# Optimization experiments

Hardware: AMD Instinct MI355X
Metric: run time of the kernel (lower is better)

The kernel has to match this reference:

```python
import jax, jax.numpy as jnp
import numpy as np

HEADS = 16
MAX_DIST = 1024

def setup_inputs() -> dict:
    key = jax.random.key(0)
    k1, k2, k3, k4 = jax.random.split(key, 4)
    b, n, dim = 2, 2048, 1024
    x = jax.random.normal(k1, (b, n, dim), dtype=jnp.float32)
    W_qkv = jax.random.normal(k2, (3 * dim, dim), dtype=jnp.float32) * (dim ** -0.5)
    W_out = jax.random.normal(k3, (dim, dim), dtype=jnp.float32) * (dim ** -0.5)
    b_out = jnp.zeros((dim,), dtype=jnp.float32)
    rel_emb = jax.random.normal(k4, (2 * MAX_DIST + 1, HEADS), dtype=jnp.float32) * 0.02
    return {"x": x, "W_qkv": W_qkv, "W_out": W_out, "b_out": b_out, "rel_emb": rel_emb}

def reference(x, W_qkv, W_out, b_out, rel_emb):
    b, n, dim = x.shape
    h = HEADS
    d = dim // h
    scale = d ** -0.5
    qkv = jnp.einsum('bnd,ed->bne', x, W_qkv)  # [b, n, 3*dim]
    q, k, v = jnp.split(qkv, 3, axis=-1)
    def to_heads(t):
        return t.reshape(b, n, h, d).transpose(0, 2, 1, 3)  # b h n d
    q, k, v = to_heads(q), to_heads(k), to_heads(v)
    # relative position bias: [1, h, n, n]
    dist = jnp.arange(n)[None, :] - jnp.arange(n)[:, None]
    idx = jnp.clip(dist, -MAX_DIST, MAX_DIST) + MAX_DIST  # [n, n]
    rel_bias = rel_emb[idx].transpose(2, 0, 1)[None]  # [1, h, n, n]
    scores = jnp.einsum('bhqd,bhkd->bhqk', q, k) * scale + rel_bias
    attn = jax.nn.softmax(scores, axis=-1)
    out = jnp.einsum('bhqk,bhkd->bhqd', attn, v)
    out = out.transpose(0, 2, 1, 3).reshape(b, n, dim)
    return jnp.einsum('bnd,ed->bne', out, W_out) + b_out
```

## Files before the change

### kernel.cpp

```cpp
#include <hip/hip_runtime.h>
#include <hip/hip_bf16.h>

typedef __attribute__((ext_vector_type(8))) short short8;
typedef __attribute__((ext_vector_type(4))) float f32x4;
typedef __attribute__((ext_vector_type(16))) float f32x16;
typedef float f32x4u __attribute__((ext_vector_type(4), aligned(4)));
typedef __attribute__((ext_vector_type(4))) unsigned short u16x4;
typedef __attribute__((ext_vector_type(2))) unsigned int u32x2;
typedef __attribute__((ext_vector_type(4))) unsigned int u32x4;
typedef __hip_bfloat16 bf16;

#define SCALE_Q 0.18033688f

#define GLD_LDS16(g, l) __builtin_amdgcn_global_load_lds(                      \
    (const __attribute__((address_space(1))) void*)(g),                        \
    (__attribute__((address_space(3))) void*)(l), 16, 0, 0)

static __device__ __forceinline__ f32x4 mfma16(short8 a, short8 b, f32x4 c) {
  return __builtin_amdgcn_mfma_f32_16x16x32_bf16(a, b, c, 0, 0, 0);
}
static __device__ __forceinline__ f32x16 mfma32(short8 a, short8 b, f32x16 c) {
  return __builtin_amdgcn_mfma_f32_32x32x16_bf16(a, b, c, 0, 0, 0);
}

static __device__ __forceinline__ unsigned cvtpk(float lo, float hi) {
  unsigned r;
  asm("v_cvt_pk_bf16_f32 %0, %1, %2" : "=v"(r) : "v"(lo), "v"(hi));
  return r;
}

static __device__ __forceinline__ float fexp2(float x) {
  float r;
  asm("v_exp_f32 %0, %1" : "=v"(r) : "v"(x));
  return r;
}

#define PLSWAP(a, b) asm("v_permlane32_swap_b32 %0, %1" : "+v"(a), "+v"(b))

__global__ __launch_bounds__(256) void k_pre(
    const float* __restrict__ x, const float* __restrict__ Wqkv,
    const float* __restrict__ Wout, const float* __restrict__ rel,
    bf16* __restrict__ xb, bf16* __restrict__ wqb, bf16* __restrict__ wob,
    float* __restrict__ relpf) {
  int bid = blockIdx.x;
  if (bid < 8192) {
    const float* in;
    bf16* out;
    long i;
    if (bid < 4096) {
      in = x; out = xb; i = (long)bid * 256 + threadIdx.x;
    } else if (bid < 7168) {
      in = Wqkv; out = wqb; i = (long)(bid - 4096) * 256 + threadIdx.x;
    } else {
      in = Wout; out = wob; i = (long)(bid - 7168) * 256 + threadIdx.x;
    }
    f32x4 v = *(const f32x4*)(in + i * 4);
    u16x4 o;
#pragma unroll
    for (int j = 0; j < 4; ++j)
      o[j] = __builtin_bit_cast(unsigned short, __float2bfloat16(v[j]));
    *(u16x4*)((unsigned short*)out + i * 4) = o;
  } else {
    int base = (bid - 8192) * 1024 + threadIdx.x;
#pragma unroll
    for (int k = 0; k < 4; ++k) {
      int i = base + k * 256;
      int h = i >> 12, ii = i & 4095;
      int dd = ii - 2047;
      dd = dd < -1024 ? -1024 : (dd > 1024 ? 1024 : dd);
      relpf[i] = rel[(size_t)(dd + 1024) * 16 + h] * 1.44269504f - 16.0f;
    }
  }
}

__global__ __launch_bounds__(256, 3) void k_gemm(
    const bf16* __restrict__ A, const bf16* __restrict__ B,
    int M, int N, int K, int epi,
    bf16* __restrict__ Qb, bf16* __restrict__ Kb, bf16* __restrict__ Vt,
    float* __restrict__ Out, const float* __restrict__ bias) {
  __shared__ bf16 lA[3][4096];
  __shared__ bf16 lB[3][4096];
  const int tid = threadIdx.x, w = tid >> 6, l = tid & 63;
  const int m0 = blockIdx.x * 128, n0 = blockIdx.y * 128;
  const int wrow = (w >> 1) * 64, wcol = (w & 1) * 64;
  const int fr = l & 15, fq = l >> 4;
  f32x4 acc[4][4] = {};
  const int c0 = w * 64 + l, c1 = c0 + 256;
  const bf16* Ag0 = A + (size_t)(m0 + (c0 >> 2)) * K + (c0 & 3) * 8;
  const bf16* Ag1 = A + (size_t)(m0 + (c1 >> 2)) * K + (c1 & 3) * 8;
  const bf16* Bg0 = B + (size_t)(n0 + (c0 >> 2)) * K + (c0 & 3) * 8;
  const bf16* Bg1 = B + (size_t)(n0 + (c1 >> 2)) * K + (c1 & 3) * 8;
  bf16* lA0 = &lA[0][w * 512];
  bf16* lA1 = &lA[0][2048 + w * 512];
  bf16* lB0 = &lB[0][w * 512];
  bf16* lB1 = &lB[0][2048 + w * 512];

#define GSTAGE(T, BI)                                                          \
  do {                                                                         \
    const int ko_ = (T) * 32;                                                  \
    GLD_LDS16(Ag0 + ko_, lA0 + (BI) * 4096);                                   \
    GLD_LDS16(Ag1 + ko_, lA1 + (BI) * 4096);                                   \
    GLD_LDS16(Bg0 + ko_, lB0 + (BI) * 4096);                                   \
    GLD_LDS16(Bg1 + ko_, lB1 + (BI) * 4096);                                   \
  } while (0)

  const int nk = K >> 5;
  GSTAGE(0, 0);
  __builtin_amdgcn_sched_barrier(0);
  GSTAGE(1, 1);
  __builtin_amdgcn_sched_barrier(0);

  int bc_ = 0, bs_ = 2;
  for (int t = 0; t < nk; ++t) {
    asm volatile("s_waitcnt vmcnt(4)" ::: "memory");
    __builtin_amdgcn_s_barrier();
    __builtin_amdgcn_sched_barrier(0);
    int tt = (t + 2 < nk) ? t + 2 : nk - 1;
    GSTAGE(tt, bs_);
    __builtin_amdgcn_sched_barrier(0);
    const bf16* pA = &lA[bc_][0];
    const bf16* pB = &lB[bc_][0];
    short8 af[4], bfv[4];
#pragma unroll
    for (int mi = 0; mi < 4; ++mi)
      af[mi] = *(const short8*)&pA[(wrow + mi * 16 + fr) * 32 + fq * 8];
#pragma unroll
    for (int ni = 0; ni < 4; ++ni)
      bfv[ni] = *(const short8*)&pB[(wcol + ni * 16 + fr) * 32 + fq * 8];
    __builtin_amdgcn_s_setprio(1);
#pragma unroll
    for (int mi = 0; mi < 4; ++mi)
#pragma unroll
      for (int ni = 0; ni < 4; ++ni)
        acc[mi][ni] = mfma16(bfv[ni], af[mi], acc[mi][ni]);
    __builtin_amdgcn_s_setprio(0);
    bc_ = (bc_ == 2) ? 0 : bc_ + 1;
    bs_ = (bs_ == 2) ? 0 : bs_ + 1;
  }
#undef GSTAGE

  if (epi == 0) {
#pragma unroll
    for (int mi = 0; mi < 4; ++mi)
#pragma unroll
      for (int ni = 0; ni < 4; ++ni) {
        int t = m0 + wrow + mi * 16 + fr;
        int e4 = n0 + wcol + ni * 16 + fq * 4;
        int sect = e4 >> 10, eh = (e4 >> 6) & 15, dh = e4 & 63;
        int b = t >> 11, tt = t & 2047;
        f32x4 a = acc[mi][ni];
        if (sect < 2) {
          size_t idx = (((size_t)b * 16 + eh) * 2048 + tt) * 64 + dh;
          float sc = (sect == 0) ? SCALE_Q : 1.f;
          u32x2 ov;
          ov[0] = cvtpk(a[0] * sc, a[1] * sc);
          ov[1] = cvtpk(a[2] * sc, a[3] * sc);
          bf16* dst = (sect == 0) ? Qb : Kb;
          *(u32x2*)(dst + idx) = ov;
        } else {
          size_t vb = ((size_t)((b << 4) + eh) * 64 + dh) * 2048 + tt;
          unsigned p0 = cvtpk(a[0], a[1]);
          unsigned p1 = cvtpk(a[2], a[3]);
          unsigned short* vp = (unsigned short*)Vt;
          vp[vb] = (unsigned short)p0;
          vp[vb + 2048] = (unsigned short)(p0 >> 16);
          vp[vb + 4096] = (unsigned short)p1;
          vp[vb + 6144] = (unsigned short)(p1 >> 16);
        }
      }
  } else {
#pragma unroll
    for (int mi = 0; mi < 4; ++mi)
#pragma unroll
      for (int ni = 0; ni < 4; ++ni) {
        int t = m0 + wrow + mi * 16 + fr;
        int e4 = n0 + wcol + ni * 16 + fq * 4;
        f32x4 bv = *(const f32x4*)(bias + e4);
        f32x4 a = acc[mi][ni];
        f32x4 o = {a[0] + bv[0], a[1] + bv[1], a[2] + bv[2], a[3] + bv[3]};
        *(f32x4*)(Out + (size_t)t * N + e4) = o;
      }
  }
}

__global__ __launch_bounds__(256, 2) void k_attn(
    const bf16* __restrict__ Qb, const bf16* __restrict__ Kb,
    const bf16* __restrict__ Vt, const float* __restrict__ relpf,
    bf16* __restrict__ AO) {
  __shared__ bf16 lK[2][8192];
  __shared__ bf16 lV[2][8192];

  const int id = blockIdx.x;
  const int xcd = id & 7, j = id >> 3;
  const int bh = xcd * 4 + (j >> 4), qt = j & 15;
  const int h = bh & 15, b = bh >> 4;
  const int tid = threadIdx.x, w = tid >> 6, l = tid & 63;
  const int r32 = l & 31, hl = l >> 5, rs7 = r32 & 7;
  const int q0w = qt * 128 + w * 32;

  const bf16* Kbh = Kb + (size_t)bh * 2048 * 64;
  const bf16* Vbh = Vt + (size_t)bh * 64 * 2048;
  const bf16* Ks[4];
  const bf16* Vs[4];
#pragma unroll
  for (int s = 0; s < 4; ++s) {
    int c = tid + 256 * s;
    int kr = c >> 3, kc = (c & 7) ^ (kr & 7);
    Ks[s] = Kbh + (size_t)kr * 64 + kc * 8;
    int vr = c >> 4, vc = (c & 15) ^ (vr & 7);
    Vs[s] = Vbh + (size_t)vr * 2048 + vc * 8;
  }

#define STAGE(KT, BI)                                                          \
  do {                                                                         \
    _Pragma("unroll") for (int s = 0; s < 4; ++s) {                            \
      GLD_LDS16(Ks[s] + (size_t)(KT) * 64, &lK[BI][(tid + 256 * s) * 8]);      \
      GLD_LDS16(Vs[s] + (KT), &lV[BI][(tid + 256 * s) * 8]);                   \
    }                                                                          \
  } while (0)

  const bf16* Qp = Qb + ((size_t)bh * 2048 + q0w + r32) * 64;
  short8 qf[4];
#pragma unroll
  for (int ks = 0; ks < 4; ++ks)
    qf[ks] = *(const short8*)(Qp + ks * 16 + hl * 8);

  const float* bp = relpf + h * 4096 + (2047 + 4 * hl - q0w - r32);

  float llane = 0.f;
  f32x16 o0 = {}, o1 = {};

  STAGE(0, 0);
  __builtin_amdgcn_sched_barrier(0);

  int cur = 0;
  for (int t = 0; t < 16; ++t) {
    const int kt = t * 128;
    asm volatile("s_waitcnt vmcnt(0)" ::: "memory");
    __builtin_amdgcn_s_barrier();
    __builtin_amdgcn_sched_barrier(0);
    f32x16 bc[4];
#pragma unroll
    for (int kb = 0; kb < 4; ++kb)
#pragma unroll
      for (int g = 0; g < 4; ++g) {
        f32x4u v = *(const f32x4u*)(bp + kt + kb * 32 + 8 * g);
#pragma unroll
        for (int e = 0; e < 4; ++e) bc[kb][g * 4 + e] = v[e];
      }
    __builtin_amdgcn_sched_barrier(0);
    if (t < 15) STAGE(kt + 128, cur ^ 1);
    __builtin_amdgcn_sched_barrier(0);
    const bf16* lKc = &lK[cur][0];
    const bf16* lVc = &lV[cur][0];
    f32x16 s[4] = {};
    __builtin_amdgcn_s_setprio(1);
#pragma unroll
    for (int kb = 0; kb < 4; ++kb)
#pragma unroll
      for (int ks = 0; ks < 4; ++ks) {
        short8 kf = *(const short8*)&lKc[(kb * 32 + r32) * 64 +
                                         (((2 * ks + hl) ^ rs7) * 8)];
        s[kb] = mfma32(kf, qf[ks], s[kb]);
      }
    __builtin_amdgcn_s_setprio(0);
    float ra[4] = {0.f, 0.f, 0.f, 0.f};
#pragma unroll
    for (int kb = 0; kb < 4; ++kb)
#pragma unroll
      for (int reg = 0; reg < 16; ++reg) {
        float e = fexp2(s[kb][reg] + bc[kb][reg]);
        s[kb][reg] = e;
        ra[reg & 3] += e;
      }
    llane += (ra[0] + ra[1]) + (ra[2] + ra[3]);
#pragma unroll
    for (int kb = 0; kb < 4; ++kb) {
#pragma unroll
      for (int kh = 0; kh < 2; ++kh) {
        const int e = kh * 8;
        unsigned a0 = cvtpk(s[kb][e + 0], s[kb][e + 1]);
        unsigned a1 = cvtpk(s[kb][e + 2], s[kb][e + 3]);
        unsigned b0 = cvtpk(s[kb][e + 4], s[kb][e + 5]);
        unsigned b1 = cvtpk(s[kb][e + 6], s[kb][e + 7]);
        PLSWAP(a0, b0);
        PLSWAP(a1, b1);
        u32x4 pw = {a0, a1, b0, b1};
        short8 pf = __builtin_bit_cast(short8, pw);
        const int ks = kb * 2 + kh;
        const int cc = ((2 * ks + hl) ^ rs7) * 8;
        short8 v0 = *(const short8*)&lVc[r32 * 128 + cc];
        short8 v1 = *(const short8*)&lVc[(32 + r32) * 128 + cc];
        __builtin_amdgcn_s_setprio(1);
        o0 = mfma32(v0, pf, o0);
        o1 = mfma32(v1, pf, o1);
        __builtin_amdgcn_s_setprio(0);
      }
    }
    cur ^= 1;
  }
#undef STAGE

  float lsum = llane + __shfl_xor(llane, 32);
  float rin = 1.f / lsum;
  bf16* aor = AO + ((size_t)(b * 2048 + q0w + r32)) * 1024 + h * 64 + hl * 4;
#pragma unroll
  for (int rg = 0; rg < 4; ++rg) {
    u32x2 ov0, ov1;
    ov0[0] = cvtpk(o0[4 * rg + 0] * rin, o0[4 * rg + 1] * rin);
    ov0[1] = cvtpk(o0[4 * rg + 2] * rin, o0[4 * rg + 3] * rin);
    *(u32x2*)(aor + rg * 8) = ov0;
    ov1[0] = cvtpk(o1[4 * rg + 0] * rin, o1[4 * rg + 1] * rin);
    ov1[1] = cvtpk(o1[4 * rg + 2] * rin, o1[4 * rg + 3] * rin);
    *(u32x2*)(aor + 32 + rg * 8) = ov1;
  }
}

extern "C" void kernel_launch(void* const* d_in, const int* in_sizes, int n_in,
                              void* d_out, int out_size, void* d_ws,
                              size_t ws_size, hipStream_t stream) {
  const float* x = (const float*)d_in[0];
  const float* Wqkv = (const float*)d_in[1];
  const float* Wout = (const float*)d_in[2];
  const float* bout = (const float*)d_in[3];
  const float* rel = (const float*)d_in[4];
  float* out = (float*)d_out;

  char* p = (char*)d_ws;
  bf16* xb  = (bf16*)(p);
  bf16* wqb = (bf16*)(p + (8ull << 20));
  bf16* wob = (bf16*)(p + (14ull << 20));
  bf16* Qb  = (bf16*)(p + (16ull << 20));
  bf16* Kb  = (bf16*)(p + (24ull << 20));
  bf16* Vtr = (bf16*)(p + (32ull << 20));
  bf16* aob = (bf16*)(p + (40ull << 20));
  float* relpf = (float*)(p + (48ull << 20));

  k_pre<<<8256, 256, 0, stream>>>(x, Wqkv, Wout, rel, xb, wqb, wob, relpf);
  k_gemm<<<dim3(32, 24), 256, 0, stream>>>(xb, wqb, 4096, 3072, 1024, 0,
                                           Qb, Kb, Vtr, nullptr, nullptr);
  k_attn<<<512, 256, 0, stream>>>(Qb, Kb, Vtr, relpf, aob);
  k_gemm<<<dim3(32, 8), 256, 0, stream>>>(aob, wob, 4096, 1024, 1024, 1,
                                          nullptr, nullptr, nullptr, out, bout);
}
```

Measured before the change: 122.3 us.

## Load K/V fragments directly from global memory instead of LDS double-buffering

```diff
diff --git a/kernel.cpp b/kernel.cpp
--- a/kernel.cpp
+++ b/kernel.cpp
@@ -187,37 +187,16 @@
     const bf16* __restrict__ Qb, const bf16* __restrict__ Kb,
     const bf16* __restrict__ Vt, const float* __restrict__ relpf,
     bf16* __restrict__ AO) {
-  __shared__ bf16 lK[2][8192];
-  __shared__ bf16 lV[2][8192];
-
   const int id = blockIdx.x;
   const int xcd = id & 7, j = id >> 3;
   const int bh = xcd * 4 + (j >> 4), qt = j & 15;
   const int h = bh & 15, b = bh >> 4;
   const int tid = threadIdx.x, w = tid >> 6, l = tid & 63;
-  const int r32 = l & 31, hl = l >> 5, rs7 = r32 & 7;
+  const int r32 = l & 31, hl = l >> 5;
   const int q0w = qt * 128 + w * 32;
 
-  const bf16* Kbh = Kb + (size_t)bh * 2048 * 64;
-  const bf16* Vbh = Vt + (size_t)bh * 64 * 2048;
-  const bf16* Ks[4];
-  const bf16* Vs[4];
-#pragma unroll
-  for (int s = 0; s < 4; ++s) {
-    int c = tid + 256 * s;
-    int kr = c >> 3, kc = (c & 7) ^ (kr & 7);
-    Ks[s] = Kbh + (size_t)kr * 64 + kc * 8;
-    int vr = c >> 4, vc = (c & 15) ^ (vr & 7);
-    Vs[s] = Vbh + (size_t)vr * 2048 + vc * 8;
-  }
-
-#define STAGE(KT, BI)                                                          \
-  do {                                                                         \
-    _Pragma("unroll") for (int s = 0; s < 4; ++s) {                            \
-      GLD_LDS16(Ks[s] + (size_t)(KT) * 64, &lK[BI][(tid + 256 * s) * 8]);      \
-      GLD_LDS16(Vs[s] + (KT), &lV[BI][(tid + 256 * s) * 8]);                   \
-    }                                                                          \
-  } while (0)
+  const bf16* Kf = Kb + (size_t)bh * 2048 * 64 + (size_t)r32 * 64 + hl * 8;
+  const bf16* Vf = Vt + (size_t)bh * 64 * 2048 + (size_t)r32 * 2048 + hl * 8;
 
   const bf16* Qp = Qb + ((size_t)bh * 2048 + q0w + r32) * 64;
   short8 qf[4];
@@ -230,49 +209,34 @@
   float llane = 0.f;
   f32x16 o0 = {}, o1 = {};
 
-  STAGE(0, 0);
-  __builtin_amdgcn_sched_barrier(0);
-
-  int cur = 0;
+#pragma unroll 1
   for (int t = 0; t < 16; ++t) {
     const int kt = t * 128;
-    asm volatile("s_waitcnt vmcnt(0)" ::: "memory");
-    __builtin_amdgcn_s_barrier();
-    __builtin_amdgcn_sched_barrier(0);
-    f32x16 bc[4];
-#pragma unroll
-    for (int kb = 0; kb < 4; ++kb)
-#pragma unroll
-      for (int g = 0; g < 4; ++g) {
-        f32x4u v = *(const f32x4u*)(bp + kt + kb * 32 + 8 * g);
-#pragma unroll
-        for (int e = 0; e < 4; ++e) bc[kb][g * 4 + e] = v[e];
-      }
-    __builtin_amdgcn_sched_barrier(0);
-    if (t < 15) STAGE(kt + 128, cur ^ 1);
-    __builtin_amdgcn_sched_barrier(0);
-    const bf16* lKc = &lK[cur][0];
-    const bf16* lVc = &lV[cur][0];
     f32x16 s[4] = {};
     __builtin_amdgcn_s_setprio(1);
 #pragma unroll
     for (int kb = 0; kb < 4; ++kb)
 #pragma unroll
       for (int ks = 0; ks < 4; ++ks) {
-        short8 kf = *(const short8*)&lKc[(kb * 32 + r32) * 64 +
-                                         (((2 * ks + hl) ^ rs7) * 8)];
+        short8 kf = *(const short8*)(Kf + (size_t)(kt + kb * 32) * 64 +
+                                     ks * 16);
         s[kb] = mfma32(kf, qf[ks], s[kb]);
       }
     __builtin_amdgcn_s_setprio(0);
     float ra[4] = {0.f, 0.f, 0.f, 0.f};
 #pragma unroll
-    for (int kb = 0; kb < 4; ++kb)
+    for (int kb = 0; kb < 4; ++kb) {
+      f32x4u bv[4];
+#pragma unroll
+      for (int g = 0; g < 4; ++g)
+        bv[g] = *(const f32x4u*)(bp + kt + kb * 32 + 8 * g);
 #pragma unroll
       for (int reg = 0; reg < 16; ++reg) {
-        float e = fexp2(s[kb][reg] + bc[kb][reg]);
+        float e = fexp2(s[kb][reg] + bv[reg >> 2][reg & 3]);
         s[kb][reg] = e;
         ra[reg & 3] += e;
       }
+    }
     llane += (ra[0] + ra[1]) + (ra[2] + ra[3]);
 #pragma unroll
     for (int kb = 0; kb < 4; ++kb) {
@@ -288,18 +252,15 @@
         u32x4 pw = {a0, a1, b0, b1};
         short8 pf = __builtin_bit_cast(short8, pw);
         const int ks = kb * 2 + kh;
-        const int cc = ((2 * ks + hl) ^ rs7) * 8;
-        short8 v0 = *(const short8*)&lVc[r32 * 128 + cc];
-        short8 v1 = *(const short8*)&lVc[(32 + r32) * 128 + cc];
+        short8 v0 = *(const short8*)(Vf + kt + ks * 16);
+        short8 v1 = *(const short8*)(Vf + 32 * 2048 + kt + ks * 16);
         __builtin_amdgcn_s_setprio(1);
         o0 = mfma32(v0, pf, o0);
         o1 = mfma32(v1, pf, o1);
         __builtin_amdgcn_s_setprio(0);
       }
     }
-    cur ^= 1;
-  }
-#undef STAGE
+  }
 
   float lsum = llane + __shfl_xor(llane, 32);
   float rin = 1.f / lsum;
```

New measurement: 211.0 us. +72.5%, slower.
